# Kernel optimization log

Measured on AMD Instinct MI355X. Metric: run time of the kernel, lower is better.

Reference implementation:

```python
import jax, jax.numpy as jnp
import numpy as np

STRIDES = (8, 16, 32, 64, 128)
LEVEL_HW = ((128, 160), (64, 80), (32, 40), (16, 20), (8, 10))
IMG_H, IMG_W = 1024, 1280
B, NUM_CLASSES = 16, 20
SCORE_THR, IOU_THR, MAX_DET = 0.05, 0.6, 1000


def _coords_all():
    # coords_fmap2orig for every level, concatenated -> [N, 2] (x, y)
    cs = []
    for (h, w), s in zip(LEVEL_HW, STRIDES):
        sx = jnp.arange(w, dtype=jnp.float32) * s + s // 2
        sy = jnp.arange(h, dtype=jnp.float32) * s + s // 2
        yy, xx = jnp.meshgrid(sy, sx, indexing='ij')
        cs.append(jnp.stack([xx.reshape(-1), yy.reshape(-1)], -1))
    return jnp.concatenate(cs, 0)


def _reshape_cat(levels):
    # list of [B,C,h,w] -> [B, sum(h*w), C]
    return jnp.concatenate(
        [p.transpose(0, 2, 3, 1).reshape(p.shape[0], -1, p.shape[1]) for p in levels], 1)


def _decode(cls_l, cnt_l, reg_l, coords):
    cls = jax.nn.sigmoid(_reshape_cat(cls_l))           # [B,N,C]
    cnt = jax.nn.sigmoid(_reshape_cat(cnt_l))[..., 0]   # [B,N]
    reg = _reshape_cat(reg_l)                           # [B,N,4] ltrb
    scores = jnp.sqrt(jnp.max(cls, -1) * cnt)           # add_centerness + sqrt
    classes = jnp.argmax(cls, -1) + 1
    boxes = jnp.concatenate([coords[None] - reg[..., :2], coords[None] + reg[..., 2:]], -1)
    return scores, classes, boxes


def _nms_keep(boxes, scores, classes, valid):
    # masked greedy per-class NMS on fixed size M; returns keep mask [M]
    boxes = jax.lax.stop_gradient(boxes)
    scores = jax.lax.stop_gradient(scores)
    maxc = jnp.max(jnp.where(valid[:, None], boxes, 0.0))
    b = boxes + (classes.astype(boxes.dtype) * (maxc + 1.0))[:, None]  # class offsets
    order = jnp.argsort(-jnp.where(valid, scores, -jnp.inf))
    b = b[order]
    v = valid[order]
    x1, y1, x2, y2 = b[:, 0], b[:, 1], b[:, 2], b[:, 3]
    areas = (x2 - x1 + 1.0) * (y2 - y1 + 1.0)
    iw = jnp.clip(jnp.minimum(x2[:, None], x2[None, :]) - jnp.maximum(x1[:, None], x1[None, :]) + 1.0, 0.0)
    ih = jnp.clip(jnp.minimum(y2[:, None], y2[None, :]) - jnp.maximum(y1[:, None], y1[None, :]) + 1.0, 0.0)
    inter = iw * ih
    iou = inter / (areas[:, None] + areas[None, :] - inter)
    M = boxes.shape[0]

    def body(i, carry):
        keep, sup = carry
        k = v[i] & (~sup[i])
        keep = keep.at[i].set(k)
        sup = sup | (k & (iou[i] > IOU_THR))
        return keep, sup

    keep_s, _ = jax.lax.fori_loop(0, M, body, (jnp.zeros(M, bool), jnp.zeros(M, bool)))
    return jnp.zeros(M, bool).at[order].set(keep_s)


def _forward(args):
    cls_r, cnt_r, reg_r = args[0:5], args[5:10], args[10:15]
    cls_i, cnt_i, reg_i = args[15:20], args[20:25], args[25:30]
    coords = _coords_all()
    s_r, c_r, b_r = _decode(cls_r, cnt_r, reg_r, coords)
    s_i, c_i, b_i = _decode(cls_i, cnt_i, reg_i, coords)
    scores = jnp.concatenate([s_r, s_i], 1)   # [B, 2N]
    classes = jnp.concatenate([c_r, c_i], 1)
    boxes = jnp.concatenate([b_r, b_i], 1)
    top_s, top_i = jax.lax.top_k(scores, MAX_DET)
    top_c = jnp.take_along_axis(classes, top_i, 1)
    top_b = jnp.take_along_axis(boxes, top_i[..., None], 1)
    valid = top_s >= SCORE_THR
    keep = jax.vmap(_nms_keep)(top_b, top_s, top_c, valid)
    # ClipBoxes: clamp to image bounds
    top_b = jnp.maximum(top_b, 0.0)
    xs = jnp.minimum(top_b[..., 0::2], IMG_W - 1.0)
    ys = jnp.minimum(top_b[..., 1::2], IMG_H - 1.0)
    top_b = jnp.stack([xs[..., 0], ys[..., 0], xs[..., 1], ys[..., 1]], -1)
    kf = keep.astype(top_s.dtype)
    return top_s * kf, top_c * keep, top_b * kf[..., None], keep


def setup_inputs() -> dict:
    key = jax.random.key(0)
    chans = {'cls': NUM_CLASSES, 'cnt': 1, 'reg': 4}
    inp = {}
    i = 0
    for mod in ('r', 'i'):
        for kind in ('cls', 'cnt', 'reg'):
            for l, (h, w) in enumerate(LEVEL_HW):
                k = jax.random.fold_in(key, i); i += 1
                inp[f'{kind}_{mod}_{l}'] = jax.random.normal(k, (B, chans[kind], h, w), jnp.float32)
    return inp


def reference(cls_r_0, cls_r_1, cls_r_2, cls_r_3, cls_r_4,
              cnt_r_0, cnt_r_1, cnt_r_2, cnt_r_3, cnt_r_4,
              reg_r_0, reg_r_1, reg_r_2, reg_r_3, reg_r_4,
              cls_i_0, cls_i_1, cls_i_2, cls_i_3, cls_i_4,
              cnt_i_0, cnt_i_1, cnt_i_2, cnt_i_3, cnt_i_4,
              reg_i_0, reg_i_1, reg_i_2, reg_i_3, reg_i_4):
    args = [cls_r_0, cls_r_1, cls_r_2, cls_r_3, cls_r_4,
            cnt_r_0, cnt_r_1, cnt_r_2, cnt_r_3, cnt_r_4,
            reg_r_0, reg_r_1, reg_r_2, reg_r_3, reg_r_4,
            cls_i_0, cls_i_1, cls_i_2, cls_i_3, cls_i_4,
            cnt_i_0, cnt_i_1, cnt_i_2, cnt_i_3, cnt_i_4,
            reg_i_0, reg_i_1, reg_i_2, reg_i_3, reg_i_4]
    return _forward(args)
```

## Files before the change

### kernel.cpp

```cpp
#include <hip/hip_runtime.h>
#include <hip/hip_bf16.h>

typedef unsigned long long u64;
typedef unsigned int u32;

#define NTOT    54560
#define NMOD    27280
#define BATCH   16
#define KPAD    1024
#define MAXD    1000
#define NBIN    16384
#define CAND    6144

struct Ptrs { const float* p[30]; };

constexpr size_t SZ_KEY   = (size_t)BATCH * NTOT * 8;
constexpr size_t SZ_TOPK  = (size_t)BATCH * KPAD * 8;
constexpr size_t SZ_TRAW  = (size_t)BATCH * KPAD * 16;
constexpr size_t SZ_T1    = (size_t)BATCH * KPAD * 4;
constexpr size_t SZ_MAXC  = (size_t)BATCH * 32 * 4;
constexpr size_t SZ_VALID = (size_t)BATCH * 32 * 4;
constexpr size_t SZ_MASK  = (size_t)BATCH * KPAD * 32 * 4;

constexpr size_t OFF_KEY    = 0;
constexpr size_t OFF_TOPK   = OFF_KEY   + SZ_KEY;
constexpr size_t OFF_TRAW   = OFF_TOPK  + SZ_TOPK;
constexpr size_t OFF_TSCORE = OFF_TRAW  + SZ_TRAW;
constexpr size_t OFF_TCLSF  = OFF_TSCORE+ SZ_T1;
constexpr size_t OFF_MAXC   = OFF_TCLSF + SZ_T1;
constexpr size_t OFF_VALID  = OFF_MAXC  + SZ_MAXC;
constexpr size_t OFF_MASK   = OFF_VALID + SZ_VALID;

__device__ inline void level_of(int nm, int& l, int& pos, int& w, int& s, int& hw) {
    if (nm < 20480)      { l = 0; pos = nm;         w = 160; s = 8;   hw = 20480; }
    else if (nm < 25600) { l = 1; pos = nm - 20480; w = 80;  s = 16;  hw = 5120; }
    else if (nm < 26880) { l = 2; pos = nm - 25600; w = 40;  s = 32;  hw = 1280; }
    else if (nm < 27200) { l = 3; pos = nm - 26880; w = 20;  s = 64;  hw = 320; }
    else                 { l = 4; pos = nm - 27200; w = 10;  s = 128; hw = 80; }
}

__device__ inline float sigm(float x) { return 1.0f / (1.0f + expf(-x)); }

__device__ inline void ld_lds16(const float* g, float* l) {
    __builtin_amdgcn_global_load_lds(
        (const __attribute__((address_space(1))) void*)g,
        (__attribute__((address_space(3))) void*)l, 16, 0, 0);
}

__global__ __launch_bounds__(128)
void decode_kernel(Ptrs ptrs, u64* __restrict__ keyAll) {
    __shared__ float lds[21 * 512];
    int cc = blockIdx.x;
    int b = blockIdx.y;

    if (cc >= 100) {
        int t = (cc - 100) * 128 + threadIdx.x;
        if (t >= 3360) return;
        int mod = t / 1680;
        int tm = t % 1680;
        int q = t & 3;
        int nm = 25600 + (tm & ~3);
        int l, pos, w, s, hw;
        level_of(nm, l, pos, w, s, hw);
        (void)w; (void)s;
        const float* clsP = ptrs.p[mod * 15 + l];
        const float* cntP = ptrs.p[mod * 15 + 5 + l];
        const float4* cb = (const float4*)(clsP + (size_t)b * 20 * hw + pos);
        int hw4 = hw >> 2;
        int c0 = q * 5;
        float4 v[5];
        #pragma unroll
        for (int c = 0; c < 5; ++c) v[c] = cb[(size_t)(c0 + c) * hw4];
        float4 cv = *(const float4*)(cntP + (size_t)b * hw + pos);
        float4 mx = v[0];
        #pragma unroll
        for (int c = 1; c < 5; ++c) {
            mx.x = fmaxf(mx.x, v[c].x); mx.y = fmaxf(mx.y, v[c].y);
            mx.z = fmaxf(mx.z, v[c].z); mx.w = fmaxf(mx.w, v[c].w);
        }
        mx.x = fmaxf(mx.x, __shfl_xor(mx.x, 1));
        mx.y = fmaxf(mx.y, __shfl_xor(mx.y, 1));
        mx.z = fmaxf(mx.z, __shfl_xor(mx.z, 1));
        mx.w = fmaxf(mx.w, __shfl_xor(mx.w, 1));
        mx.x = fmaxf(mx.x, __shfl_xor(mx.x, 2));
        mx.y = fmaxf(mx.y, __shfl_xor(mx.y, 2));
        mx.z = fmaxf(mx.z, __shfl_xor(mx.z, 2));
        mx.w = fmaxf(mx.w, __shfl_xor(mx.w, 2));
        float ma = (q & 1) ? ((q & 2) ? mx.w : mx.y) : ((q & 2) ? mx.z : mx.x);
        float ca = (q & 1) ? ((q & 2) ? cv.w : cv.y) : ((q & 2) ? cv.z : cv.x);
        u32 sb = __float_as_uint(sqrtf(__fmul_rn(sigm(ma), sigm(ca))));
        int n = mod * NMOD + nm + q;
        keyAll[(size_t)b * NTOT + n] = ((u64)sb << 16) | (u64)(65535 - n);
        return;
    }

    int mod = cc / 50, c = cc % 50;
    int l     = (c < 40) ? 0 : 1;
    int hw    = (c < 40) ? 20480 : 5120;
    int pos0  = (c < 40) ? c * 512 : (c - 40) * 512;
    int nmb   = (l == 0) ? pos0 : 20480 + pos0;
    const float* clsP = ptrs.p[mod * 15 + l];
    const float* cntP = ptrs.p[mod * 15 + 5 + l];
    int wave = threadIdx.x >> 6, lane = threadIdx.x & 63;

    const float* cbase = clsP + (size_t)b * 20 * hw + pos0 + wave * 256 + lane * 4;
    float* dbase = lds + wave * 256;
    #pragma unroll
    for (int ch = 0; ch < 20; ++ch)
        ld_lds16(cbase + (size_t)ch * hw, dbase + ch * 512);
    ld_lds16(cntP + (size_t)b * hw + pos0 + wave * 256 + lane * 4, dbase + 20 * 512);
    __syncthreads();

    int t = threadIdx.x;
    const float4* l4 = (const float4*)lds;
    float4 mx = l4[t];
    #pragma unroll
    for (int ch = 1; ch < 20; ++ch) {
        float4 v = l4[ch * 128 + t];
        mx.x = fmaxf(mx.x, v.x); mx.y = fmaxf(mx.y, v.y);
        mx.z = fmaxf(mx.z, v.z); mx.w = fmaxf(mx.w, v.w);
    }
    float4 cv = l4[20 * 128 + t];

    int n = mod * NMOD + nmb + t * 4;
    u32 s0 = __float_as_uint(sqrtf(__fmul_rn(sigm(mx.x), sigm(cv.x))));
    u32 s1 = __float_as_uint(sqrtf(__fmul_rn(sigm(mx.y), sigm(cv.y))));
    u32 s2 = __float_as_uint(sqrtf(__fmul_rn(sigm(mx.z), sigm(cv.z))));
    u32 s3 = __float_as_uint(sqrtf(__fmul_rn(sigm(mx.w), sigm(cv.w))));
    ulonglong2* ka2 = (ulonglong2*)(keyAll + (size_t)b * NTOT + n);
    ulonglong2 k01, k23;
    k01.x = ((u64)s0 << 16) | (u64)(65535 - n);
    k01.y = ((u64)s1 << 16) | (u64)(65535 - (n + 1));
    k23.x = ((u64)s2 << 16) | (u64)(65535 - (n + 2));
    k23.y = ((u64)s3 << 16) | (u64)(65535 - (n + 3));
    ka2[0] = k01; ka2[1] = k23;
}

__global__ __launch_bounds__(1024)
void select_kernel(const u64* __restrict__ keyAll, u64* __restrict__ topkey,
                   u32* __restrict__ maxcG) {
    int b = blockIdx.x, tid = threadIdx.x;
    int lane = tid & 63, wid = tid >> 6;
    __shared__ u32 shist[NBIN];
    __shared__ u64 scand[CAND];
    __shared__ u64 stopk[KPAD];
    __shared__ u32 warep[16];
    __shared__ int sB1;

    if (tid == 0) maxcG[b * 32] = 0u;
    #pragma unroll
    for (int j = 0; j < NBIN / 1024; ++j) shist[tid + j * 1024] = 0u;
    __syncthreads();

    const u64* keys = keyAll + (size_t)b * NTOT;
    const u64 SENT = ~0ull;
    for (int n0 = 0; n0 < NTOT; n0 += 8192) {
        u64 kk[8];
        #pragma unroll
        for (int r = 0; r < 8; ++r) {
            int idx = n0 + r * 1024 + tid;
            kk[r] = (idx < NTOT) ? keys[idx] : SENT;
        }
        #pragma unroll
        for (int r = 0; r < 8; ++r)
            if (kk[r] != SENT) atomicAdd(&shist[(u32)(kk[r] >> 32)], 1u);
    }
    __syncthreads();

    u32 loc[16]; u32 sum = 0;
    #pragma unroll
    for (int j = 0; j < 16; ++j) { loc[j] = shist[NBIN - 1 - (tid * 16 + j)]; sum += loc[j]; }
    u32 v = sum;
    #pragma unroll
    for (int off = 1; off < 64; off <<= 1) {
        u32 t2 = (u32)__shfl_up((int)v, off);
        if (lane >= off) v += t2;
    }
    if (lane == 63) warep[wid] = v;
    __syncthreads();
    if (tid < 16) {
        u32 p = warep[tid];
        #pragma unroll
        for (int off = 1; off < 16; off <<= 1) {
            u32 t2 = (u32)__shfl_up((int)p, off);
            if (tid >= off) p += t2;
        }
        warep[tid] = p;
    }
    __syncthreads();
    u32 incl = v + (wid ? warep[wid - 1] : 0u);
    u32 excl = incl - sum;
    if (excl < (u32)MAXD && incl >= (u32)MAXD) {
        u32 c = excl;
        #pragma unroll
        for (int j = 0; j < 16; ++j) {
            c += loc[j];
            if (c >= (u32)MAXD) { sB1 = NBIN - 1 - (tid * 16 + j); break; }
        }
    }
    u32 run = excl;
    #pragma unroll
    for (int j = 0; j < 16; ++j) {
        int bin = NBIN - 1 - (tid * 16 + j);
        shist[bin] = run;
        run += loc[j];
    }
    __syncthreads();
    int B1 = sB1;

    for (int n0 = 0; n0 < NTOT; n0 += 8192) {
        u64 kk[8];
        #pragma unroll
        for (int r = 0; r < 8; ++r) {
            int idx = n0 + r * 1024 + tid;
            kk[r] = (idx < NTOT) ? keys[idx] : 0ull;
        }
        #pragma unroll
        for (int r = 0; r < 8; ++r) {
            if (kk[r] != 0ull && (int)(kk[r] >> 32) >= B1) {
                u32 p = atomicAdd(&shist[(u32)(kk[r] >> 32)], 1u);
                if (p < CAND) scand[p] = kk[r];
            }
        }
    }
    __syncthreads();
    int Ctot = min((int)shist[B1], CAND);

    for (int i = tid; i < Ctot; i += 1024) {
        u64 ki = scand[i];
        int bin = (int)(ki >> 32);
        int st = (int)shist[bin + 1];
        int en = min((int)shist[bin], Ctot);
        int pos = st;
        for (int j = st; j < en; ++j) pos += (scand[j] > ki) ? 1 : 0;
        if (pos < MAXD) stopk[pos] = ki;
    }
    __syncthreads();
    if (tid < MAXD) topkey[(size_t)b * KPAD + tid] = stopk[tid];
}

__global__ __launch_bounds__(128)
void gather_kernel(Ptrs ptrs, const u64* __restrict__ topkey,
                   float4* __restrict__ traw, float* __restrict__ tscore,
                   float* __restrict__ tclsf, u32* __restrict__ validwords,
                   u32* __restrict__ maxcG) {
    #pragma clang fp contract(off)
    int b = blockIdx.y;
    int tid = threadIdx.x;
    int half = tid & 1;
    int i = blockIdx.x * 64 + (tid >> 1);
    int active = (i < MAXD);

    float score = 0.f;
    float best = -1.0f; int bi = 0;
    float ra = 0.f, rb2 = 0.f;
    int pos = 0, w = 1, s = 0;
    if (active) {
        u64 key = topkey[(size_t)b * KPAD + i];
        int n = 65535 - (int)(key & 0xFFFFull);
        score = __uint_as_float((u32)(key >> 16));
        int mod = (n >= NMOD) ? 1 : 0;
        int nm = n - mod * NMOD;
        int l, hw;
        level_of(nm, l, pos, w, s, hw);
        const float* clsP = ptrs.p[mod * 15 + l];
        const float* regP = ptrs.p[mod * 15 + 10 + l];
        const float* cbp = clsP + (size_t)b * 20 * hw + pos;
        const float* rbp = regP + (size_t)b * 4 * hw + pos;
        float cl[10];
        int c0 = half * 10;
        #pragma unroll
        for (int c = 0; c < 10; ++c) cl[c] = cbp[(size_t)(c0 + c) * hw];
        ra  = rbp[(size_t)(half * 2) * hw];
        rb2 = rbp[(size_t)(half * 2 + 1) * hw];
        #pragma unroll
        for (int c = 0; c < 10; ++c) {
            float p = sigm(cl[c]);
            if (p > best) { best = p; bi = c0 + c; }
        }
    }
    float po  = __shfl_xor(best, 1);
    int   bio = __shfl_xor(bi, 1);
    float rao = __shfl_xor(ra, 1);
    float rbo = __shfl_xor(rb2, 1);
    if (half == 0) { if (po > best)  { best = po; bi = bio; } }
    else           { if (po >= best) { best = po; bi = bio; } }
    float clsf = active ? (float)(bi + 1) : 0.f;
    float r0 = half ? rao : ra,  r1 = half ? rbo : rb2;
    float r2 = half ? ra  : rao, r3 = half ? rb2 : rbo;

    float4 bx = make_float4(0.f, 0.f, 0.f, 0.f);
    if (active) {
        int xi = pos % w, yi = pos / w;
        float cx = (float)(xi * s + (s >> 1));
        float cy = (float)(yi * s + (s >> 1));
        bx.x = cx - r0; bx.y = cy - r1; bx.z = cx + r2; bx.w = cy + r3;
    }
    int valid = active && (score >= 0.05f) && (half == 0);
    float contrib = valid ? fmaxf(0.0f, fmaxf(fmaxf(bx.x, bx.y), fmaxf(bx.z, bx.w))) : 0.0f;
    float red = contrib;
    #pragma unroll
    for (int off = 32; off > 0; off >>= 1) red = fmaxf(red, __shfl_down(red, off));
    if ((tid & 63) == 0) atomicMax(&maxcG[b * 32], __float_as_uint(red));
    u64 ball = __ballot(valid != 0);
    if ((tid & 63) == 0) {
        u32 word = 0;
        for (int j = 0; j < 32; ++j) word |= (u32)((ball >> (2 * j)) & 1ull) << j;
        validwords[b * 32 + blockIdx.x * 2 + (tid >> 6)] = word;
    }
    if (half == 0) {
        size_t oo = (size_t)b * KPAD + i;
        traw[oo] = bx; tscore[oo] = score; tclsf[oo] = clsf;
    }
}

#define SW(t) ((((t) & 31) << 3) | ((t) >> 5))
__global__ __launch_bounds__(256)
void mask_kernel(const float4* __restrict__ traw, const float* __restrict__ tclsf,
                 const u32* __restrict__ maxcG, u32* __restrict__ maskG) {
    #pragma clang fp contract(off)
    int u = blockIdx.x, b = blockIdx.y, tid = threadIdx.x;
    int g, wg;
    if (u < 32)      { g = u >> 2;              wg = u & 3; }
    else if (u < 56) { int d = u - 32; g = 8  + d / 3;        wg = 1 + d % 3; }
    else if (u < 72) { int d = u - 56; g = 16 + (d >> 1);     wg = 2 + (d & 1); }
    else             { g = 24 + (u - 72);       wg = 3; }
    int i0 = g * 32, j0 = wg * 256;
    float m1 = __uint_as_float(maxcG[b * 32]) + 1.0f;

    __shared__ float cx1[256], cy1[256], cx2[256], cy2[256], ca[256];
    {
        int t = tid;
        float4 f = traw[(size_t)b * KPAD + j0 + t];
        float o = __fmul_rn(tclsf[(size_t)b * KPAD + j0 + t], m1);
        float ox1 = __fadd_rn(f.x, o), oy1 = __fadd_rn(f.y, o);
        float ox2 = __fadd_rn(f.z, o), oy2 = __fadd_rn(f.w, o);
        float dw = ox2 - ox1 + 1.0f;
        float dh = oy2 - oy1 + 1.0f;
        int ts = SW(t);
        cx1[ts] = ox1; cy1[ts] = oy1; cx2[ts] = ox2; cy2[ts] = oy2;
        ca[ts] = __fmul_rn(dw, dh);
    }
    __syncthreads();

    int ir = tid >> 3, wr = tid & 7;
    int i = i0 + ir;
    float4 fi = traw[(size_t)b * KPAD + i];
    float oi = __fmul_rn(tclsf[(size_t)b * KPAD + i], m1);
    float ix1 = __fadd_rn(fi.x, oi), iy1 = __fadd_rn(fi.y, oi);
    float ix2 = __fadd_rn(fi.z, oi), iy2 = __fadd_rn(fi.w, oi);
    float dwi = ix2 - ix1 + 1.0f, dhi = iy2 - iy1 + 1.0f;
    float ai = __fmul_rn(dwi, dhi);
    u32 bits = 0;
    int jb = wr * 32;
    for (int jj = 0; jj < 32; ++jj) {
        int js = SW(jb + jj);
        float iw = fminf(ix2, cx2[js]) - fmaxf(ix1, cx1[js]) + 1.0f;
        iw = fmaxf(iw, 0.0f);
        float ih = fminf(iy2, cy2[js]) - fmaxf(iy1, cy1[js]) + 1.0f;
        ih = fmaxf(ih, 0.0f);
        float inter = iw * ih;
        float denom = (ai + ca[js]) - inter;
        float iou = inter / denom;
        bits |= (iou > 0.6f) ? (1u << jj) : 0u;
    }
    maskG[((size_t)b * KPAD + i) * 32 + wg * 8 + wr] = bits;
}

__global__ __launch_bounds__(512)
void scan_out_kernel(const u32* __restrict__ maskG, const u32* __restrict__ validbits,
                     const float4* __restrict__ traw, const float* __restrict__ tscore,
                     const float* __restrict__ tclsf, float* __restrict__ out) {
    __shared__ u32 sm[KPAD * 32];
    __shared__ u32 keeps[32];
    int b = blockIdx.x, tid = threadIdx.x;

    const uint4* s4 = (const uint4*)(maskG + (size_t)b * KPAD * 32);
    uint4* d4 = (uint4*)sm;
    #pragma unroll
    for (int r = 0; r < 16; ++r) d4[tid + r * 512] = s4[tid + r * 512];
    __syncthreads();

    if (tid < 64) {
        int lane = tid, lw = lane & 31;
        u32 vreg = (lane < 32) ? validbits[b * 32 + lane] : 0u;
        u32 removed = 0u, keepw = 0u;
        u32 mA[8], mB[8];
        #pragma unroll
        for (int d = 0; d < 8; ++d) {
            mA[d] = sm[d * 32 + lw];
            mB[d] = sm[(d + 8) * 32 + lw];
        }
        auto step8 = [&](int base, u32* ms) {
            #pragma unroll
            for (int d = 0; d < 8; ++d) {
                int i = base + d;
                int wi = i >> 5, bi2 = i & 31;
                u32 rw = (u32)__builtin_amdgcn_readlane((int)removed, wi);
                u32 vw = (u32)__builtin_amdgcn_readlane((int)vreg, wi);
                u32 k = ((vw >> bi2) & 1u) & (~(rw >> bi2) & 1u);
                if (k) removed |= ms[d];
                if (lane == wi) keepw |= (k << bi2);
                ms[d] = sm[(i + 16) * 32 + lw];
            }
        };
        for (int t = 0; t < 62; ++t) { step8(t * 16, mA); step8(t * 16 + 8, mB); }
        step8(992, mA);
        if (lane < 32) keeps[lane] = keepw;
    }
    __syncthreads();

    const int BQ = BATCH * MAXD;
    for (int s2 = tid; s2 < MAXD; s2 += 512) {
        u32 kf = (keeps[s2 >> 5] >> (s2 & 31)) & 1u;
        size_t oo = (size_t)b * KPAD + s2;
        float score = tscore[oo];
        float clsf = tclsf[oo];
        float4 bx = traw[oo];
        float x1 = fminf(fmaxf(bx.x, 0.f), 1279.f);
        float y1 = fminf(fmaxf(bx.y, 0.f), 1023.f);
        float x2 = fminf(fmaxf(bx.z, 0.f), 1279.f);
        float y2 = fminf(fmaxf(bx.w, 0.f), 1023.f);
        int base = b * MAXD + s2;
        out[base] = kf ? score : 0.0f;
        out[BQ + base] = kf ? clsf : 0.0f;
        float* ob = out + 2 * BQ + (size_t)base * 4;
        ob[0] = kf ? x1 : 0.f; ob[1] = kf ? y1 : 0.f;
        ob[2] = kf ? x2 : 0.f; ob[3] = kf ? y2 : 0.f;
        out[6 * BQ + base] = kf ? 1.0f : 0.0f;
    }
}

extern "C" void kernel_launch(void* const* d_in, const int* in_sizes, int n_in,
                              void* d_out, int out_size, void* d_ws, size_t ws_size,
                              hipStream_t stream) {
    Ptrs ptrs;
    for (int i = 0; i < 30; ++i) ptrs.p[i] = (const float*)d_in[i];

    char* ws = (char*)d_ws;
    u64*    keyAll    = (u64*)   (ws + OFF_KEY);
    u64*    topkey    = (u64*)   (ws + OFF_TOPK);
    float4* traw      = (float4*)(ws + OFF_TRAW);
    float*  tscore    = (float*) (ws + OFF_TSCORE);
    float*  tclsf     = (float*) (ws + OFF_TCLSF);
    u32*    maxcG     = (u32*)   (ws + OFF_MAXC);
    u32*    validbits = (u32*)   (ws + OFF_VALID);
    u32*    maskG     = (u32*)   (ws + OFF_MASK);
    float*  out       = (float*)d_out;

    decode_kernel<<<dim3(127, BATCH), 128, 0, stream>>>(ptrs, keyAll);
    select_kernel<<<BATCH, 1024, 0, stream>>>(keyAll, topkey, maxcG);
    gather_kernel<<<dim3(16, BATCH), 128, 0, stream>>>(ptrs, topkey, traw, tscore, tclsf,
                                                       validbits, maxcG);
    mask_kernel<<<dim3(80, BATCH), 256, 0, stream>>>(traw, tclsf, maxcG, maskG);
    scan_out_kernel<<<BATCH, 512, 0, stream>>>(maskG, validbits, traw, tscore, tclsf, out);
}
```

Before: 250.4 us.

## Block the greedy NMS scan into 32-row groups with a swizzled shared layout

Replaces the serial per-row greedy NMS scan, which did a dependent readlane and shared-memory load for each of 1024 rows, with a blocked scan. Each 32-row group first resolves suppression inside the group using its diagonal mask word broadcast by readlane. It then ORs the kept rows' mask words into the removed vector, with the two half-wavefronts splitting the 32 rows and merging through a shuffle. The shared-memory copy of the mask is XOR-swizzled to avoid bank conflicts on the column-style reads of the diagonal word. This shortens the serial dependency chain, at the cost of more shared loads per group and extra index arithmetic.

Result: faster. 236.3 us (-5.6%).

```diff
diff --git a/kernel.cpp b/kernel.cpp
--- a/kernel.cpp
+++ b/kernel.cpp
@@ -378,35 +378,47 @@
     const uint4* s4 = (const uint4*)(maskG + (size_t)b * KPAD * 32);
     uint4* d4 = (uint4*)sm;
     #pragma unroll
-    for (int r = 0; r < 16; ++r) d4[tid + r * 512] = s4[tid + r * 512];
+    for (int r = 0; r < 16; ++r) {
+        int w4 = tid + r * 512;
+        int row = w4 >> 3, c4 = w4 & 7;
+        d4[(row << 3) | (c4 ^ (row & 7))] = s4[w4];
+    }
     __syncthreads();
 
     if (tid < 64) {
         int lane = tid, lw = lane & 31;
-        u32 vreg = (lane < 32) ? validbits[b * 32 + lane] : 0u;
+        int rbase = (lane >> 5) << 4;
+        u32 vword = validbits[b * 32 + lw];
         u32 removed = 0u, keepw = 0u;
-        u32 mA[8], mB[8];
-        #pragma unroll
-        for (int d = 0; d < 8; ++d) {
-            mA[d] = sm[d * 32 + lw];
-            mB[d] = sm[(d + 8) * 32 + lw];
-        }
-        auto step8 = [&](int base, u32* ms) {
+        for (int g = 0; g < 32; ++g) {
+            int i0 = g << 5;
+            u32 intra = sm[((i0 + lw) << 5) | (g ^ ((lw & 7) << 2))];
+            u32 remg = (u32)__builtin_amdgcn_readlane((int)removed, g);
+            u32 valg = (u32)__builtin_amdgcn_readlane((int)vword, g);
+            u32 cand = valg & ~remg;
+            u32 keep32 = 0u, sup = 0u;
             #pragma unroll
-            for (int d = 0; d < 8; ++d) {
-                int i = base + d;
-                int wi = i >> 5, bi2 = i & 31;
-                u32 rw = (u32)__builtin_amdgcn_readlane((int)removed, wi);
-                u32 vw = (u32)__builtin_amdgcn_readlane((int)vreg, wi);
-                u32 k = ((vw >> bi2) & 1u) & (~(rw >> bi2) & 1u);
-                if (k) removed |= ms[d];
-                if (lane == wi) keepw |= (k << bi2);
-                ms[d] = sm[(i + 16) * 32 + lw];
+            for (int i = 0; i < 32; ++i) {
+                u32 mi = (u32)__builtin_amdgcn_readlane((int)intra, i);
+                u32 kb = cand & ~sup & (1u << i);
+                sup |= kb ? mi : 0u;
+                keep32 |= kb;
             }
-        };
-        for (int t = 0; t < 62; ++t) { step8(t * 16, mA); step8(t * 16 + 8, mB); }
-        step8(992, mA);
-        if (lane < 32) keeps[lane] = keepw;
+            u32 ksh = keep32 >> rbase;
+            u32 acc0 = 0u, acc1 = 0u;
+            #pragma unroll
+            for (int r = 0; r < 16; r += 2) {
+                u32 r0 = sm[((i0 + rbase + r)     << 5) | (lw ^ ((r & 7) << 2))];
+                u32 r1 = sm[((i0 + rbase + r + 1) << 5) | (lw ^ (((r + 1) & 7) << 2))];
+                acc0 |= ((ksh >> r) & 1u)       ? r0 : 0u;
+                acc1 |= ((ksh >> (r + 1)) & 1u) ? r1 : 0u;
+            }
+            u32 acc = acc0 | acc1;
+            acc |= (u32)__shfl_xor((int)acc, 32);
+            removed |= acc;
+            if (lw == g) keepw = keep32;
+        }
+        if (lane < 32) keeps[lw] = keepw;
     }
     __syncthreads();
 
```
